# Performance work log

Hardware: AMD Instinct MI355X
Metric: run time of the kernel (lower is better)

## Reference

```python
import jax, jax.numpy as jnp
import numpy as np

B, T, C, H = 2, 2048, 1024, 16
HD = C // H          # head_dim = 64
RD = HD // 2         # rotary half-dim = 32


def _rope_tables(T, rd, base=10000.0):
    inv_freq = 1.0 / (base ** (np.arange(rd, dtype=np.float32) / rd))
    t = np.arange(T, dtype=np.float32)
    ang = np.outer(t, inv_freq)  # [T, rd]
    cos = np.cos(ang)[None, :, None, :]  # [1,T,1,rd]
    sin = np.sin(ang)[None, :, None, :]
    return jnp.asarray(cos), jnp.asarray(sin)


def setup_inputs() -> dict:
    key = jax.random.key(0)
    k1, k2, k3 = jax.random.split(key, 3)
    cos, sin = _rope_tables(T, RD)
    return {
        "x": jax.random.normal(k1, (B, T, C), dtype=jnp.float32),
        "cos": cos,
        "sin": sin,
        "W_qkv": jax.random.normal(k2, (C, C), dtype=jnp.float32) / np.sqrt(C),
        "W_proj": jax.random.normal(k3, (C, C), dtype=jnp.float32) / np.sqrt(C),
        "window_left": 512,
    }


def _apply_rotary(x, cos, sin):
    # x: [B,T,H,HD]
    x1, x2 = x[..., :RD], x[..., RD:]
    y1 = x1 * cos + x2 * sin
    y2 = -x1 * sin + x2 * cos
    return jnp.concatenate([y1, y2], axis=-1)


def _rms_norm(x):
    eps = jnp.finfo(x.dtype).eps
    ms = jnp.mean(jnp.square(x), axis=-1, keepdims=True)
    return x * jax.lax.rsqrt(ms + eps)


def reference(x, cos, sin, W_qkv, W_proj, window_left):
    Bx, Tx, Cx = x.shape
    scale = HD ** -0.5
    # tied QKV projection (single matmul)
    w = jnp.einsum("btc,cd->btd", x, W_qkv).reshape(Bx, Tx, H, HD)
    w = _apply_rotary(w, cos, sin)
    w = _rms_norm(w)                      # [B,T,H,HD]
    wq = jnp.transpose(w, (0, 2, 1, 3))    # [B,H,T,HD]
    dots = jnp.einsum("bhqd,bhkd->bhqk", wq, wq) * scale  # [B,H,T,T]
    # causal + sliding-window mask: allow 0 <= (q - k) <= window_left
    i = jnp.arange(Tx)[:, None]
    j = jnp.arange(Tx)[None, :]
    dist = i - j
    allowed = (dist >= 0) & ((window_left <= 0) | (dist <= window_left))
    dots = jnp.where(allowed, dots, -jnp.inf)
    attn = jax.nn.softmax(dots, axis=-1)
    out = jnp.einsum("bhqk,bhkd->bhqd", attn, wq)
    out = jnp.transpose(out, (0, 2, 1, 3)).reshape(Bx, Tx, Cx)
    return jnp.einsum("btc,cd->btd", out, W_proj)
```

## Files before the change

### kernel.cpp

```cpp
#include <hip/hip_runtime.h>
#include <hip/hip_bf16.h>

typedef __bf16 bf16_t;
typedef __bf16 bf16x4 __attribute__((ext_vector_type(4)));
typedef __bf16 bf16x8 __attribute__((ext_vector_type(8)));
typedef float f32x4 __attribute__((ext_vector_type(4)));

#define B_ 2
#define T_ 2048
#define C_ 1024
#define H_ 16
#define HD_ 64
#define RD_ 32
#define M_ (B_ * T_)

__global__ __launch_bounds__(256) void k_prep(const float* __restrict__ x,
                                              bf16_t* __restrict__ xb,
                                              const float* __restrict__ Wq,
                                              bf16_t* __restrict__ wqt,
                                              const float* __restrict__ Wp,
                                              bf16_t* __restrict__ wpt) {
    const int bid = blockIdx.x;
    if (bid < 4096) {
        int i = bid * 256 + threadIdx.x;
        float4 v = reinterpret_cast<const float4*>(x)[i];
        bf16x4 o;
        o[0] = (bf16_t)v.x; o[1] = (bf16_t)v.y; o[2] = (bf16_t)v.z; o[3] = (bf16_t)v.w;
        reinterpret_cast<bf16x4*>(xb)[i] = o;
    } else {
        __shared__ float tile[32][33];
        int b2 = bid - 4096;
        const float* W = (b2 < 1024) ? Wq : Wp;
        bf16_t* Wt = (b2 < 1024) ? wqt : wpt;
        b2 &= 1023;
        const int n0 = (b2 & 31) * 32, k0 = (b2 >> 5) * 32;
        const int tx = threadIdx.x & 31, ty = threadIdx.x >> 5;
        for (int i = ty; i < 32; i += 8)
            tile[i][tx] = W[(size_t)(k0 + i) * C_ + n0 + tx];
        __syncthreads();
        for (int i = ty; i < 32; i += 8)
            Wt[(size_t)(n0 + i) * C_ + k0 + tx] = (bf16_t)tile[tx][i];
    }
}

template <bool FUSED>
__global__ __launch_bounds__(256) void k_gemm(const bf16_t* __restrict__ A,
                                              const bf16_t* __restrict__ Bt,
                                              float* __restrict__ C,
                                              const float* __restrict__ ct,
                                              const float* __restrict__ st,
                                              bf16_t* __restrict__ qp,
                                              bf16_t* __restrict__ vp,
                                              int M, int N, int K) {
    constexpr int SMEM_BYTES = FUSED ? 52224 : 49152;
    __shared__ __align__(16) char smem[SMEM_BYTES];
    bf16_t* As = (bf16_t*)smem;
    bf16_t* Bs = (bf16_t*)(smem + 32768);
    const int tid = threadIdx.x;
    const int lane = tid & 63, w = tid >> 6;
    const int wr = w >> 1, wc = w & 1;
    const int g = lane >> 4, li = lane & 15;
    const int bid = blockIdx.x;
    const int work = (bid & 7) * 64 + (bid >> 3);
    const int bx = work & 15;
    const int by = work >> 4;
    const size_t rowA0 = (size_t)by * 128;
    const size_t colB0 = (size_t)bx * 64;
    const bf16_t* Ab = A + rowA0 * K;
    const bf16_t* Bb = Bt + colB0 * K;
    f32x4 acc[4][2] = {};

    const int lr = lane >> 3;
    const int swc = ((lane & 7) ^ lr) * 8;

    auto stage = [&](int buf, int k0) {
        bf16_t* Ad = As + buf * 8192 + (w * 8) * 64;
        bf16_t* Bd = Bs + buf * 4096 + (w * 8) * 64;
#pragma unroll
        for (int a = 0; a < 4; ++a) {
            const bf16_t* src = Ab + (size_t)(a * 32 + w * 8 + lr) * K + k0 + swc;
            __builtin_amdgcn_global_load_lds(
                (const __attribute__((address_space(1))) void*)src,
                (__attribute__((address_space(3))) void*)(Ad + a * 32 * 64), 16, 0, 0);
        }
#pragma unroll
        for (int bq = 0; bq < 2; ++bq) {
            const bf16_t* src = Bb + (size_t)(bq * 32 + w * 8 + lr) * K + k0 + swc;
            __builtin_amdgcn_global_load_lds(
                (const __attribute__((address_space(1))) void*)src,
                (__attribute__((address_space(3))) void*)(Bd + bq * 32 * 64), 16, 0, 0);
        }
    };

    stage(0, 0);
    __syncthreads();
    int cur = 0;
    const int NT = K >> 6;
    for (int kt = 0; kt < NT; ++kt) {
        if (kt < NT - 1) stage(cur ^ 1, (kt + 1) << 6);
        bf16x8 af[4][2], bfr[2][2];
#pragma unroll
        for (int i = 0; i < 4; ++i) {
            const int row = wr * 64 + i * 16 + li;
#pragma unroll
            for (int kk = 0; kk < 2; ++kk)
                af[i][kk] = *(const bf16x8*)(As + cur * 8192 + row * 64 +
                                             (((kk * 4 + g) ^ (li & 7)) * 8));
        }
#pragma unroll
        for (int j = 0; j < 2; ++j) {
            const int row = wc * 32 + j * 16 + li;
#pragma unroll
            for (int kk = 0; kk < 2; ++kk)
                bfr[j][kk] = *(const bf16x8*)(Bs + cur * 4096 + row * 64 +
                                              (((kk * 4 + g) ^ (li & 7)) * 8));
        }
#pragma unroll
        for (int i = 0; i < 4; ++i)
#pragma unroll
            for (int j = 0; j < 2; ++j)
#pragma unroll
                for (int kk = 0; kk < 2; ++kk)
                    acc[i][j] = __builtin_amdgcn_mfma_f32_16x16x32_bf16(
                        af[i][kk], bfr[j][kk], acc[i][j], 0, 0, 0);
        __syncthreads();
        cur ^= 1;
    }

    if constexpr (!FUSED) {
#pragma unroll
        for (int i = 0; i < 4; ++i)
#pragma unroll
            for (int j = 0; j < 2; ++j)
#pragma unroll
                for (int r = 0; r < 4; ++r) {
                    size_t row = rowA0 + wr * 64 + i * 16 + g * 4 + r;
                    size_t col = colB0 + wc * 32 + j * 16 + li;
                    C[row * N + col] = acc[i][j][r];
                }
    } else {
        float* ot = (float*)smem;
        bf16_t* qs = (bf16_t*)(smem + 34816);
#pragma unroll
        for (int i = 0; i < 4; ++i)
#pragma unroll
            for (int j = 0; j < 2; ++j)
#pragma unroll
                for (int r = 0; r < 4; ++r)
                    ot[(wr * 64 + i * 16 + g * 4 + r) * 68 + wc * 32 + j * 16 + li] =
                        acc[i][j][r];
        __syncthreads();
        const int bb = (int)(rowA0 >> 11);
        {
            const int row = tid >> 1, half = tid & 1;
            const int t = ((int)rowA0 + row) & 2047;
            const float* own = ot + row * 68 + half * 32;
            const float* par = ot + row * 68 + (half ^ 1) * 32;
            const float* cp = ct + (size_t)t * RD_;
            const float* sp = st + (size_t)t * RD_;
            float y[32];
            float sq = 0.f;
#pragma unroll
            for (int c4 = 0; c4 < 8; ++c4) {
                float4 xo = ((const float4*)own)[c4];
                float4 xp = ((const float4*)par)[c4];
                float4 cc = ((const float4*)cp)[c4];
                float4 ss = ((const float4*)sp)[c4];
                float* yy = y + c4 * 4;
                if (half == 0) {
                    yy[0] = xo.x * cc.x + xp.x * ss.x;
                    yy[1] = xo.y * cc.y + xp.y * ss.y;
                    yy[2] = xo.z * cc.z + xp.z * ss.z;
                    yy[3] = xo.w * cc.w + xp.w * ss.w;
                } else {
                    yy[0] = xo.x * cc.x - xp.x * ss.x;
                    yy[1] = xo.y * cc.y - xp.y * ss.y;
                    yy[2] = xo.z * cc.z - xp.z * ss.z;
                    yy[3] = xo.w * cc.w - xp.w * ss.w;
                }
                sq += yy[0] * yy[0] + yy[1] * yy[1] + yy[2] * yy[2] + yy[3] * yy[3];
            }
            sq += __shfl_xor(sq, 1);
            const float rn = rsqrtf(sq * (1.0f / 64.0f) + 1.1920929e-7f);
            bf16_t yb[32];
#pragma unroll
            for (int e = 0; e < 32; ++e) yb[e] = (bf16_t)(y[e] * rn);
            bf16_t* qpb = qp + ((size_t)(bb * H_ + bx) * 128 + (t >> 4)) * 1024;
#pragma unroll
            for (int c8 = 0; c8 < 4; ++c8) {
                const int chunk = (half * 4 + c8) * 16 + (t & 15);
                *(bf16x8*)(qpb + chunk * 8) = *(const bf16x8*)(yb + c8 * 8);
            }
#pragma unroll
            for (int e = 0; e < 32; ++e)
                qs[(half * 32 + e) * 136 + row] = yb[e];
        }
        __syncthreads();
        {
            const int d = tid >> 2, jc4 = tid & 3;
            const int tt0 = (int)((rowA0 & 2047) >> 6);
            bf16_t* vpb = vp + ((size_t)(bb * H_ + bx) * 32) * 4096;
#pragma unroll
            for (int c = 0; c < 4; ++c) {
                const int jc = jc4 * 4 + c;
                bf16x8 v8 = *(const bf16x8*)(qs + d * 136 + jc * 8);
                bf16_t* dst = vpb + (size_t)(tt0 + (jc >> 3)) * 4096 +
                              ((d >> 4) * 8 + (jc & 7)) * 128 + (d & 15) * 8;
                *(bf16x8*)dst = v8;
            }
        }
    }
}

__global__ __launch_bounds__(256, 2) void k_attn(const bf16_t* __restrict__ qp,
                                                 const bf16_t* __restrict__ vp,
                                                 bf16_t* __restrict__ aout,
                                                 const int* __restrict__ wlp) {
    __shared__ bf16_t pb[4][16][40];
    const int tid = threadIdx.x;
    const int lane = tid & 63, w = tid >> 6;
    const int g = lane >> 4, li = lane & 15;
    const int bid = blockIdx.x;
    const int work = (bid & 7) * 128 + (bid >> 3);
    const int tb = work & 31;
    const int h = (work >> 5) & 15;
    const int b = work >> 9;
    const int Q0 = tb * 64;
    const bf16_t* bq = qp + (size_t)(b * H_ + h) * 131072;
    const bf16_t* bv = vp + (size_t)(b * H_ + h) * 131072;
    const int wl = wlp[0];
    const int wle = (wl <= 0 || wl > T_) ? T_ : wl;
    const int qw = Q0 + w * 16;
    const int qg = qw + li;

    const int fo = (g * 16 + li) * 8;
    const int vo = g * 128 + li * 8;

    bf16x8 aq[2];
    aq[0] = *(const bf16x8*)(bq + (size_t)(qw >> 4) * 1024 + fo);
    aq[1] = *(const bf16x8*)(bq + (size_t)(qw >> 4) * 1024 + fo + 512);

    f32x4 o[4] = {};
    float m = -1e30f, l = 0.f;
    const float SC = 0.125f * 1.44269504089f;

    const int kb0 = (qw > wle) ? ((qw - wle) >> 6) : 0;
    const int kb1 = qw >> 6;

    for (int kb = kb0; kb <= kb1; ++kb) {
        const int J0 = kb << 6;
        const bf16_t* kt = bq + (size_t)kb * 4096;
        const bf16_t* vt = bv + (size_t)kb * 4096;
        bf16x8 kf[2][4];
#pragma unroll
        for (int ks = 0; ks < 2; ++ks)
#pragma unroll
            for (int nb = 0; nb < 4; ++nb)
                kf[ks][nb] = *(const bf16x8*)(kt + nb * 1024 + ks * 512 + fo);
        f32x4 s4[4] = {};
        __builtin_amdgcn_s_setprio(1);
#pragma unroll
        for (int ks = 0; ks < 2; ++ks)
#pragma unroll
            for (int nb = 0; nb < 4; ++nb)
                s4[nb] = __builtin_amdgcn_mfma_f32_16x16x32_bf16(kf[ks][nb], aq[ks],
                                                                 s4[nb], 0, 0, 0);
        __builtin_amdgcn_s_setprio(0);
        bf16x8 vf[2][4];
#pragma unroll
        for (int ks = 0; ks < 2; ++ks)
#pragma unroll
            for (int dnb = 0; dnb < 4; ++dnb)
                vf[ks][dnb] = *(const bf16x8*)(vt + dnb * 1024 + ks * 512 + vo);
        float sv[4][4];
        float mn = m;
#pragma unroll
        for (int nb = 0; nb < 4; ++nb)
#pragma unroll
            for (int r = 0; r < 4; ++r) {
                const int j = J0 + nb * 16 + g * 4 + r;
                const int dist = qg - j;
                float x = s4[nb][r] * SC;
                sv[nb][r] = (dist >= 0 && dist <= wle) ? x : -__builtin_inff();
                mn = fmaxf(mn, sv[nb][r]);
            }
        mn = fmaxf(mn, __shfl_xor(mn, 16));
        mn = fmaxf(mn, __shfl_xor(mn, 32));
        const float al = exp2f(m - mn);
        m = mn;
        float la = 0.f;
#pragma unroll
        for (int nb = 0; nb < 4; ++nb)
#pragma unroll
            for (int r = 0; r < 4; ++r) {
                float pv = exp2f(sv[nb][r] - m);
                sv[nb][r] = pv;
                la += pv;
            }
        la += __shfl_xor(la, 16);
        la += __shfl_xor(la, 32);
        l = l * al + la;
        float alq[4];
#pragma unroll
        for (int r = 0; r < 4; ++r) alq[r] = __shfl(al, g * 4 + r);
#pragma unroll
        for (int dnb = 0; dnb < 4; ++dnb)
#pragma unroll
            for (int r = 0; r < 4; ++r) o[dnb][r] *= alq[r];
#pragma unroll
        for (int ks = 0; ks < 2; ++ks) {
#pragma unroll
            for (int nb2 = 0; nb2 < 2; ++nb2) {
                const int nb = ks * 2 + nb2;
                bf16x4 pk;
                pk[0] = (bf16_t)sv[nb][0]; pk[1] = (bf16_t)sv[nb][1];
                pk[2] = (bf16_t)sv[nb][2]; pk[3] = (bf16_t)sv[nb][3];
                *reinterpret_cast<bf16x4*>(&pb[w][li][nb2 * 16 + g * 4]) = pk;
            }
            bf16x8 pa = *reinterpret_cast<const bf16x8*>(&pb[w][li][g * 8]);
            __builtin_amdgcn_s_setprio(1);
#pragma unroll
            for (int dnb = 0; dnb < 4; ++dnb)
                o[dnb] = __builtin_amdgcn_mfma_f32_16x16x32_bf16(pa, vf[ks][dnb],
                                                                 o[dnb], 0, 0, 0);
            __builtin_amdgcn_s_setprio(0);
        }
    }

    const float rli = 1.0f / l;
    float rlq[4];
#pragma unroll
    for (int r = 0; r < 4; ++r) rlq[r] = __shfl(rli, g * 4 + r);
#pragma unroll
    for (int dnb = 0; dnb < 4; ++dnb)
#pragma unroll
        for (int r = 0; r < 4; ++r) {
            size_t t = (size_t)qw + g * 4 + r;
            aout[((size_t)b * T_ + t) * C_ + h * 64 + dnb * 16 + li] =
                (bf16_t)(o[dnb][r] * rlq[r]);
        }
}

extern "C" void kernel_launch(void* const* d_in, const int* in_sizes, int n_in,
                              void* d_out, int out_size, void* d_ws, size_t ws_size,
                              hipStream_t stream) {
    const float* x     = (const float*)d_in[0];
    const float* ct    = (const float*)d_in[1];
    const float* st    = (const float*)d_in[2];
    const float* Wqkv  = (const float*)d_in[3];
    const float* Wproj = (const float*)d_in[4];
    const int*   wl    = (const int*)d_in[5];
    float* out = (float*)d_out;
    char* ws = (char*)d_ws;

    bf16_t* xb    = (bf16_t*)(ws);
    bf16_t* wqkvt = (bf16_t*)(ws + (8ull << 20));
    bf16_t* wprot = (bf16_t*)(ws + (10ull << 20));
    bf16_t* qp    = (bf16_t*)(ws + (12ull << 20));
    bf16_t* vp    = (bf16_t*)(ws + (20ull << 20));
    bf16_t* ao    = (bf16_t*)(ws + (28ull << 20));

    k_prep<<<dim3(6144), dim3(256), 0, stream>>>(x, xb, Wqkv, wqkvt, Wproj, wprot);
    k_gemm<true><<<dim3(512), dim3(256), 0, stream>>>(xb, wqkvt, nullptr, ct, st,
                                                      qp, vp, M_, C_, C_);
    k_attn<<<dim3(1024), dim3(256), 0, stream>>>(qp, vp, ao, wl);
    k_gemm<false><<<dim3(512), dim3(256), 0, stream>>>(ao, wprot, out, nullptr, nullptr,
                                                       nullptr, nullptr, M_, C_, C_);
}
```

Before: 69.32 us.

## Process two 16-query row groups per wave in attention to reuse K/V fragments

Each wave in the attention kernel now handles 32 query rows, as two 16-row groups, instead of 16. The K and V fragments loaded for each key block feed MFMAs for both groups, so K/V global loads per query are halved. Each group keeps its own online-softmax state, and the attention grid shrinks from 1024 to 512 blocks. In exchange, register pressure and per-wave serial work go up, and there are fewer blocks, which may lower occupancy and worsen load balance.

Result: no change. 70.14 us (+1.2%).

```diff
diff --git a/kernel.cpp b/kernel.cpp
--- a/kernel.cpp
+++ b/kernel.cpp
@@ -216,36 +216,69 @@
                                                  const bf16_t* __restrict__ vp,
                                                  bf16_t* __restrict__ aout,
                                                  const int* __restrict__ wlp) {
-    __shared__ bf16_t pb[4][16][40];
+    __shared__ bf16_t pb[4][2][16][40];
     const int tid = threadIdx.x;
     const int lane = tid & 63, w = tid >> 6;
     const int g = lane >> 4, li = lane & 15;
     const int bid = blockIdx.x;
-    const int work = (bid & 7) * 128 + (bid >> 3);
-    const int tb = work & 31;
-    const int h = (work >> 5) & 15;
-    const int b = work >> 9;
-    const int Q0 = tb * 64;
+    const int work = (bid & 7) * 64 + (bid >> 3);
+    const int tb = work & 15;
+    const int h = (work >> 4) & 15;
+    const int b = work >> 8;
+    const int Q0 = tb * 128;
     const bf16_t* bq = qp + (size_t)(b * H_ + h) * 131072;
     const bf16_t* bv = vp + (size_t)(b * H_ + h) * 131072;
     const int wl = wlp[0];
     const int wle = (wl <= 0 || wl > T_) ? T_ : wl;
-    const int qw = Q0 + w * 16;
-    const int qg = qw + li;
+    const int qw = Q0 + w * 32;
+    const int qgA = qw + li;
+    const int qgB = qw + 16 + li;
 
     const int fo = (g * 16 + li) * 8;
     const int vo = g * 128 + li * 8;
 
-    bf16x8 aq[2];
-    aq[0] = *(const bf16x8*)(bq + (size_t)(qw >> 4) * 1024 + fo);
-    aq[1] = *(const bf16x8*)(bq + (size_t)(qw >> 4) * 1024 + fo + 512);
-
-    f32x4 o[4] = {};
-    float m = -1e30f, l = 0.f;
+    bf16x8 aqA0 = *(const bf16x8*)(bq + (size_t)(qw >> 4) * 1024 + fo);
+    bf16x8 aqA1 = *(const bf16x8*)(bq + (size_t)(qw >> 4) * 1024 + fo + 512);
+    bf16x8 aqB0 = *(const bf16x8*)(bq + (size_t)((qw >> 4) + 1) * 1024 + fo);
+    bf16x8 aqB1 = *(const bf16x8*)(bq + (size_t)((qw >> 4) + 1) * 1024 + fo + 512);
+
+    f32x4 oA[4] = {}, oB[4] = {};
+    float mA = -1e30f, lA = 0.f, mB = -1e30f, lB = 0.f;
     const float SC = 0.125f * 1.44269504089f;
 
     const int kb0 = (qw > wle) ? ((qw - wle) >> 6) : 0;
     const int kb1 = qw >> 6;
+
+#define SOFTMAX_G(S4, QG, M, L, O)                                                     \
+    {                                                                                  \
+        float mn = M;                                                                  \
+        _Pragma("unroll") for (int nb = 0; nb < 4; ++nb)                               \
+        _Pragma("unroll") for (int r = 0; r < 4; ++r) {                                \
+            const int j = J0 + nb * 16 + g * 4 + r;                                    \
+            const int dist = (QG) - j;                                                 \
+            float x = S4[nb][r] * SC;                                                  \
+            S4[nb][r] = (dist >= 0 && dist <= wle) ? x : -__builtin_inff();            \
+            mn = fmaxf(mn, S4[nb][r]);                                                 \
+        }                                                                              \
+        mn = fmaxf(mn, __shfl_xor(mn, 16));                                            \
+        mn = fmaxf(mn, __shfl_xor(mn, 32));                                            \
+        const float al = exp2f(M - mn);                                                \
+        M = mn;                                                                        \
+        float la = 0.f;                                                                \
+        _Pragma("unroll") for (int nb = 0; nb < 4; ++nb)                               \
+        _Pragma("unroll") for (int r = 0; r < 4; ++r) {                                \
+            float pv = exp2f(S4[nb][r] - M);                                           \
+            S4[nb][r] = pv;                                                            \
+            la += pv;                                                                  \
+        }                                                                              \
+        la += __shfl_xor(la, 16);                                                      \
+        la += __shfl_xor(la, 32);                                                      \
+        L = L * al + la;                                                               \
+        float alq[4];                                                                  \
+        _Pragma("unroll") for (int r = 0; r < 4; ++r) alq[r] = __shfl(al, g * 4 + r);  \
+        _Pragma("unroll") for (int dnb = 0; dnb < 4; ++dnb)                            \
+        _Pragma("unroll") for (int r = 0; r < 4; ++r) O[dnb][r] *= alq[r];             \
+    }
 
     for (int kb = kb0; kb <= kb1; ++kb) {
         const int J0 = kb << 6;
@@ -257,14 +290,19 @@
 #pragma unroll
             for (int nb = 0; nb < 4; ++nb)
                 kf[ks][nb] = *(const bf16x8*)(kt + nb * 1024 + ks * 512 + fo);
-        f32x4 s4[4] = {};
+        f32x4 s4A[4] = {}, s4B[4] = {};
         __builtin_amdgcn_s_setprio(1);
 #pragma unroll
         for (int ks = 0; ks < 2; ++ks)
 #pragma unroll
-            for (int nb = 0; nb < 4; ++nb)
-                s4[nb] = __builtin_amdgcn_mfma_f32_16x16x32_bf16(kf[ks][nb], aq[ks],
-                                                                 s4[nb], 0, 0, 0);
+            for (int nb = 0; nb < 4; ++nb) {
+                bf16x8 aq0 = (ks == 0) ? aqA0 : aqA1;
+                bf16x8 bq0 = (ks == 0) ? aqB0 : aqB1;
+                s4A[nb] = __builtin_amdgcn_mfma_f32_16x16x32_bf16(kf[ks][nb], aq0,
+                                                                  s4A[nb], 0, 0, 0);
+                s4B[nb] = __builtin_amdgcn_mfma_f32_16x16x32_bf16(kf[ks][nb], bq0,
+                                                                  s4B[nb], 0, 0, 0);
+            }
         __builtin_amdgcn_s_setprio(0);
         bf16x8 vf[2][4];
 #pragma unroll
@@ -272,72 +310,55 @@
 #pragma unroll
             for (int dnb = 0; dnb < 4; ++dnb)
                 vf[ks][dnb] = *(const bf16x8*)(vt + dnb * 1024 + ks * 512 + vo);
-        float sv[4][4];
-        float mn = m;
-#pragma unroll
-        for (int nb = 0; nb < 4; ++nb)
-#pragma unroll
-            for (int r = 0; r < 4; ++r) {
-                const int j = J0 + nb * 16 + g * 4 + r;
-                const int dist = qg - j;
-                float x = s4[nb][r] * SC;
-                sv[nb][r] = (dist >= 0 && dist <= wle) ? x : -__builtin_inff();
-                mn = fmaxf(mn, sv[nb][r]);
-            }
-        mn = fmaxf(mn, __shfl_xor(mn, 16));
-        mn = fmaxf(mn, __shfl_xor(mn, 32));
-        const float al = exp2f(m - mn);
-        m = mn;
-        float la = 0.f;
-#pragma unroll
-        for (int nb = 0; nb < 4; ++nb)
-#pragma unroll
-            for (int r = 0; r < 4; ++r) {
-                float pv = exp2f(sv[nb][r] - m);
-                sv[nb][r] = pv;
-                la += pv;
-            }
-        la += __shfl_xor(la, 16);
-        la += __shfl_xor(la, 32);
-        l = l * al + la;
-        float alq[4];
-#pragma unroll
-        for (int r = 0; r < 4; ++r) alq[r] = __shfl(al, g * 4 + r);
-#pragma unroll
-        for (int dnb = 0; dnb < 4; ++dnb)
-#pragma unroll
-            for (int r = 0; r < 4; ++r) o[dnb][r] *= alq[r];
+
+        SOFTMAX_G(s4A, qgA, mA, lA, oA)
+        SOFTMAX_G(s4B, qgB, mB, lB, oB)
+
 #pragma unroll
         for (int ks = 0; ks < 2; ++ks) {
 #pragma unroll
             for (int nb2 = 0; nb2 < 2; ++nb2) {
                 const int nb = ks * 2 + nb2;
-                bf16x4 pk;
-                pk[0] = (bf16_t)sv[nb][0]; pk[1] = (bf16_t)sv[nb][1];
-                pk[2] = (bf16_t)sv[nb][2]; pk[3] = (bf16_t)sv[nb][3];
-                *reinterpret_cast<bf16x4*>(&pb[w][li][nb2 * 16 + g * 4]) = pk;
-            }
-            bf16x8 pa = *reinterpret_cast<const bf16x8*>(&pb[w][li][g * 8]);
+                bf16x4 pkA, pkB;
+                pkA[0] = (bf16_t)s4A[nb][0]; pkA[1] = (bf16_t)s4A[nb][1];
+                pkA[2] = (bf16_t)s4A[nb][2]; pkA[3] = (bf16_t)s4A[nb][3];
+                pkB[0] = (bf16_t)s4B[nb][0]; pkB[1] = (bf16_t)s4B[nb][1];
+                pkB[2] = (bf16_t)s4B[nb][2]; pkB[3] = (bf16_t)s4B[nb][3];
+                *reinterpret_cast<bf16x4*>(&pb[w][0][li][nb2 * 16 + g * 4]) = pkA;
+                *reinterpret_cast<bf16x4*>(&pb[w][1][li][nb2 * 16 + g * 4]) = pkB;
+            }
+            bf16x8 paA = *reinterpret_cast<const bf16x8*>(&pb[w][0][li][g * 8]);
+            bf16x8 paB = *reinterpret_cast<const bf16x8*>(&pb[w][1][li][g * 8]);
             __builtin_amdgcn_s_setprio(1);
 #pragma unroll
-            for (int dnb = 0; dnb < 4; ++dnb)
-                o[dnb] = __builtin_amdgcn_mfma_f32_16x16x32_bf16(pa, vf[ks][dnb],
-                                                                 o[dnb], 0, 0, 0);
+            for (int dnb = 0; dnb < 4; ++dnb) {
+                oA[dnb] = __builtin_amdgcn_mfma_f32_16x16x32_bf16(paA, vf[ks][dnb],
+                                                                  oA[dnb], 0, 0, 0);
+                oB[dnb] = __builtin_amdgcn_mfma_f32_16x16x32_bf16(paB, vf[ks][dnb],
+                                                                  oB[dnb], 0, 0, 0);
+            }
             __builtin_amdgcn_s_setprio(0);
         }
     }
-
-    const float rli = 1.0f / l;
-    float rlq[4];
-#pragma unroll
-    for (int r = 0; r < 4; ++r) rlq[r] = __shfl(rli, g * 4 + r);
+#undef SOFTMAX_G
+
+    const float rlA = 1.0f / lA, rlB = 1.0f / lB;
+    float rlqA[4], rlqB[4];
+#pragma unroll
+    for (int r = 0; r < 4; ++r) {
+        rlqA[r] = __shfl(rlA, g * 4 + r);
+        rlqB[r] = __shfl(rlB, g * 4 + r);
+    }
 #pragma unroll
     for (int dnb = 0; dnb < 4; ++dnb)
 #pragma unroll
         for (int r = 0; r < 4; ++r) {
-            size_t t = (size_t)qw + g * 4 + r;
-            aout[((size_t)b * T_ + t) * C_ + h * 64 + dnb * 16 + li] =
-                (bf16_t)(o[dnb][r] * rlq[r]);
+            const size_t tA = (size_t)qw + g * 4 + r;
+            const size_t tB = tA + 16;
+            aout[((size_t)b * T_ + tA) * C_ + h * 64 + dnb * 16 + li] =
+                (bf16_t)(oA[dnb][r] * rlqA[r]);
+            aout[((size_t)b * T_ + tB) * C_ + h * 64 + dnb * 16 + li] =
+                (bf16_t)(oB[dnb][r] * rlqB[r]);
         }
 }
 
@@ -363,7 +384,7 @@
     k_prep<<<dim3(6144), dim3(256), 0, stream>>>(x, xb, Wqkv, wqkvt, Wproj, wprot);
     k_gemm<true><<<dim3(512), dim3(256), 0, stream>>>(xb, wqkvt, nullptr, ct, st,
                                                       qp, vp, M_, C_, C_);
-    k_attn<<<dim3(1024), dim3(256), 0, stream>>>(qp, vp, ao, wl);
+    k_attn<<<dim3(512), dim3(256), 0, stream>>>(qp, vp, ao, wl);
     k_gemm<false><<<dim3(512), dim3(256), 0, stream>>>(ao, wprot, out, nullptr, nullptr,
                                                        nullptr, nullptr, M_, C_, C_);
 }
```
